# Optimization experiments

Measured on AMD Instinct MI355X. Metric: run time of the kernel, lower is better.

The kernel has to match this reference:

```python
import jax, jax.numpy as jnp
import numpy as np
import math

B, S, IN_DIM = 8, 1024, 64
OUT_DIM, NB = 128, 6
LN_EPS = 1e-5

def setup_inputs() -> dict:
    key = jax.random.key(0)
    k1, k2, k3, k4 = jax.random.split(key, 4)
    seq = jax.random.normal(k1, (B, S, IN_DIM), dtype=jnp.float32)
    # torch inits: M ~ U(-0.5,0.5), P ~ U(-0.1,0.1), residual_proj.weight ~ U(-0.1,0.1)
    M = jax.random.uniform(k2, (OUT_DIM, IN_DIM), minval=-0.5, maxval=0.5, dtype=jnp.float32)
    P = jax.random.uniform(k3, (OUT_DIM, OUT_DIM, NB), minval=-0.1, maxval=0.1, dtype=jnp.float32)
    res_W = jax.random.uniform(k4, (OUT_DIM, IN_DIM), minval=-0.1, maxval=0.1, dtype=jnp.float32)
    gamma = jnp.ones((OUT_DIM,), dtype=jnp.float32)
    beta = jnp.zeros((OUT_DIM,), dtype=jnp.float32)
    return {"seq": seq, "M": M, "P": P, "res_W": res_W, "gamma": gamma, "beta": beta}

def _layer(x, M, P, res_W, gamma, beta):
    b, s, _ = x.shape
    out_dim, _, nb = P.shape
    # x_trans = x @ M.T then LayerNorm over last dim
    x_t = jnp.einsum('bsj,ij->bsi', x, M)  # (b,s,out)
    mu = jnp.mean(x_t, axis=-1, keepdims=True)
    var = jnp.mean((x_t - mu) ** 2, axis=-1, keepdims=True)
    x_n = (x_t - mu) * jax.lax.rsqrt(var + LN_EPS) * gamma + beta
    # periods[i,j,g] = i*(out*nb) + j*nb + g + 2
    periods = (jnp.arange(out_dim * out_dim * nb, dtype=jnp.float32) + 2.0).reshape(out_dim, out_dim, nb)
    pos = jnp.arange(s, dtype=jnp.float32)
    phi = jnp.cos((2.0 * math.pi) * pos[:, None, None, None] / periods[None])  # (s,out,out,nb)
    # Nk[b,s,i] = sum_{j,g} P[i,j,g] * x_n[b,s,j] * phi[s,i,j,g]
    W = jnp.einsum('ijg,sijg->sij', P, phi)      # (s,out,out) position-dependent mixing
    Nk = jnp.einsum('bsj,sij->bsi', x_n, W)      # (b,s,out)
    residual = jnp.einsum('bsj,ij->bsi', x, res_W)  # 'separate' residual projection
    return Nk + residual

def reference(seq, M, P, res_W, gamma, beta):
    return _layer(seq, M, P, res_W, gamma, beta)
```

## Files before the change

kernel.cpp:

```cpp
#include <hip/hip_runtime.h>
#include <math.h>

#define BD 8
#define SD 1024
#define ID 64
#define OD 128
#define NBD 6
#define TI 4
#define SCH 32
#define SS 8
#define WPAD 136

typedef short bf16x8 __attribute__((ext_vector_type(8)));
typedef float f32x4 __attribute__((ext_vector_type(4)));
typedef ushort ushortx8 __attribute__((ext_vector_type(8)));

__device__ __forceinline__ ushort rne_bf16(float f) {
    union { float f; unsigned u; } cv; cv.f = f;
    return (ushort)((cv.u + 0x7FFFu + ((cv.u >> 16) & 1u)) >> 16);
}
__device__ __forceinline__ float bf16_to_f(ushort u) {
    union { unsigned u; float f; } cv; cv.u = ((unsigned)u) << 16;
    return cv.f;
}

__device__ __forceinline__ bf16x8 pack8(float4 a, float4 b) {
    union { ushort u[8]; bf16x8 v; } p;
    p.u[0] = rne_bf16(a.x); p.u[1] = rne_bf16(a.y);
    p.u[2] = rne_bf16(a.z); p.u[3] = rne_bf16(a.w);
    p.u[4] = rne_bf16(b.x); p.u[5] = rne_bf16(b.y);
    p.u[6] = rne_bf16(b.z); p.u[7] = rne_bf16(b.w);
    return p.v;
}

__device__ __forceinline__ void pack8_split(float4 a, float4 b,
                                            bf16x8* hi, bf16x8* lo) {
    union { ushort u[8]; bf16x8 v; } ph, pl;
    const float e[8] = {a.x, a.y, a.z, a.w, b.x, b.y, b.z, b.w};
    #pragma unroll
    for (int k = 0; k < 8; ++k) {
        const ushort h = rne_bf16(e[k]);
        ph.u[k] = h;
        pl.u[k] = rne_bf16(e[k] - bf16_to_f(h));
    }
    *hi = ph.v; *lo = pl.v;
}

__global__ __launch_bounds__(256) void ln_mfma(
    const float* __restrict__ seq,
    const float* __restrict__ M,
    const float* __restrict__ resW,
    const float* __restrict__ gamma,
    const float* __restrict__ beta,
    ushort* __restrict__ xnT,
    float* __restrict__ out)
{
    const int t  = threadIdx.x;
    const int s0 = blockIdx.x * 2;
    const int w  = t >> 6;
    const int l  = t & 63;
    const int lr = l & 15;
    const int lk = l >> 4;

    __shared__ float Ct[16][132];

    bf16x8 ahi[2], alo[2];
    {
        const int ba = lr & 7, sa = lr >> 3;
        const float* __restrict__ arow = &seq[(ba * SD + s0 + sa) * ID];
        #pragma unroll
        for (int ka = 0; ka < 2; ++ka) {
            const float4 v0 = *(const float4*)&arow[ka * 32 + lk * 8];
            const float4 v1 = *(const float4*)&arow[ka * 32 + lk * 8 + 4];
            pack8_split(v0, v1, &ahi[ka], &alo[ka]);
        }
    }
    bf16x8 bfr[2][2][2];
    #pragma unroll
    for (int mat = 0; mat < 2; ++mat) {
        const float* __restrict__ Wm = mat ? resW : M;
        #pragma unroll
        for (int ct = 0; ct < 2; ++ct) {
            const float* __restrict__ wrow = &Wm[(w * 32 + ct * 16 + lr) * ID];
            #pragma unroll
            for (int kb = 0; kb < 2; ++kb) {
                const float4 v0 = *(const float4*)&wrow[kb * 32 + lk * 8];
                const float4 v1 = *(const float4*)&wrow[kb * 32 + lk * 8 + 4];
                bfr[mat][ct][kb] = pack8(v0, v1);
            }
        }
    }

    f32x4 accx[2], accr[2];
    #pragma unroll
    for (int ct = 0; ct < 2; ++ct) {
        f32x4 a4 = {0.f, 0.f, 0.f, 0.f};
        a4 = __builtin_amdgcn_mfma_f32_16x16x32_bf16(alo[0], bfr[0][ct][0], a4, 0, 0, 0);
        a4 = __builtin_amdgcn_mfma_f32_16x16x32_bf16(alo[1], bfr[0][ct][1], a4, 0, 0, 0);
        a4 = __builtin_amdgcn_mfma_f32_16x16x32_bf16(ahi[0], bfr[0][ct][0], a4, 0, 0, 0);
        a4 = __builtin_amdgcn_mfma_f32_16x16x32_bf16(ahi[1], bfr[0][ct][1], a4, 0, 0, 0);
        accx[ct] = a4;
        f32x4 r4 = {0.f, 0.f, 0.f, 0.f};
        r4 = __builtin_amdgcn_mfma_f32_16x16x32_bf16(ahi[0], bfr[1][ct][0], r4, 0, 0, 0);
        r4 = __builtin_amdgcn_mfma_f32_16x16x32_bf16(ahi[1], bfr[1][ct][1], r4, 0, 0, 0);
        accr[ct] = r4;
    }

    #pragma unroll
    for (int ct = 0; ct < 2; ++ct)
        #pragma unroll
        for (int q = 0; q < 4; ++q) {
            const int r = lk * 4 + q;
            const int b = r & 7, sl = r >> 3;
            out[(b * SD + s0 + sl) * OD + w * 32 + ct * 16 + lr] = accr[ct][q];
        }
    #pragma unroll
    for (int ct = 0; ct < 2; ++ct)
        #pragma unroll
        for (int q = 0; q < 4; ++q)
            Ct[lk * 4 + q][w * 32 + ct * 16 + lr] = accx[ct][q];
    __syncthreads();

    {
        const int row = t >> 4;
        const int c0  = (t & 15) * 8;
        float sum = 0.f, ssq = 0.f;
        #pragma unroll
        for (int e = 0; e < 8; ++e) {
            const float v = Ct[row][c0 + e];
            sum += v; ssq = fmaf(v, v, ssq);
        }
        #pragma unroll
        for (int m = 1; m < 16; m <<= 1) {
            sum += __shfl_xor(sum, m, 64);
            ssq += __shfl_xor(ssq, m, 64);
        }
        const float mu   = sum * (1.0f / OD);
        const float vr   = ssq * (1.0f / OD) - mu * mu;
        const float rstd = rsqrtf(vr + 1e-5f);

        const float4 g0 = *(const float4*)&gamma[c0];
        const float4 g1 = *(const float4*)&gamma[c0 + 4];
        const float4 b0 = *(const float4*)&beta[c0];
        const float4 b1 = *(const float4*)&beta[c0 + 4];
        const float gv[8] = {g0.x,g0.y,g0.z,g0.w,g1.x,g1.y,g1.z,g1.w};
        const float bv[8] = {b0.x,b0.y,b0.z,b0.w,b1.x,b1.y,b1.z,b1.w};

        union { ushort u[8]; ushortx8 v; } xo;
        #pragma unroll
        for (int e = 0; e < 8; ++e) {
            const float xv = (Ct[row][c0 + e] - mu) * rstd * gv[e] + bv[e];
            xo.u[e] = rne_bf16(xv);
        }
        const int b  = row & 7, sl = row >> 3;
        *(ushortx8*)&xnT[((s0 + sl) * BD + b) * OD + c0] = xo.v;
    }
}

__global__ __launch_bounds__(512, 6) void nk_kernel(
    const float* __restrict__ P,
    const ushort* __restrict__ xnT,
    float* __restrict__ out)
{
    const int sc = blockIdx.x;
    const int i0 = blockIdx.y * TI;
    const int t  = threadIdx.x;
    const int iw = t >> 7;
    const int jb = t & 127;
    const int wv = t >> 6;
    const int l  = t & 63;

    __shared__ ushort Wl[SS][TI][WPAD];
    __shared__ ushort Xl[SS][BD][WPAD];
    __shared__ float  Cst[SS][BD][TI];

    float Pv[NBD], kk[NBD], c0[NBD], c1[NBD];
    const int ig = i0 + iw;
    const float s0f = (float)(sc * SCH);
    #pragma unroll
    for (int g = 0; g < NBD; ++g) {
        Pv[g] = P[(ig * OD + jb) * NBD + g];
        const float per = (float)(ig * (OD * NBD) + jb * NBD + g + 2);
        const float rp  = __builtin_amdgcn_rcpf(per);
        kk[g] = 2.0f * __builtin_amdgcn_cosf(rp);
        c1[g] = __builtin_amdgcn_cosf(__builtin_amdgcn_fractf(s0f * rp));
        c0[g] = __builtin_amdgcn_cosf(__builtin_amdgcn_fractf((s0f - 1.0f) * rp));
    }

    for (int u = 0; u < SCH / SS; ++u) {
        const int sb = sc * SCH + u * SS;
        {
            const uint4* __restrict__ src = (const uint4*)(xnT + sb * (BD * OD));
            #pragma unroll
            for (int r = 0; r < 2; ++r) {
                const int e  = t + 512 * r;
                const uint4 v = src[e];
                const int eo = e << 3;
                const int si = eo >> 10;
                const int b  = (eo >> 7) & 7;
                const int j0 = eo & 127;
                *(uint4*)&Xl[si][b][j0] = v;
            }
        }
        #pragma unroll
        for (int ssi = 0; ssi < SS; ++ssi) {
            float wvv = 0.f;
            #pragma unroll
            for (int g = 0; g < NBD; ++g) wvv = fmaf(Pv[g], c1[g], wvv);
            #pragma unroll
            for (int g = 0; g < NBD; ++g) {
                const float cn = fmaf(kk[g], c1[g], -c0[g]);
                c0[g] = c1[g]; c1[g] = cn;
            }
            Wl[ssi][iw][jb] = rne_bf16(wvv);
        }
        __syncthreads();
        {
            f32x4 acc4 = {0.f, 0.f, 0.f, 0.f};
            #pragma unroll
            for (int m = 0; m < 4; ++m) {
                const bf16x8 a = *(const bf16x8*)&Xl[wv][l & 7][m * 32 + (l >> 4) * 8];
                const bf16x8 b = *(const bf16x8*)&Wl[wv][l & 3][m * 32 + (l >> 4) * 8];
                acc4 = __builtin_amdgcn_mfma_f32_16x16x32_bf16(a, b, acc4, 0, 0, 0);
            }
            const int col  = l & 15;
            const int rowg = l >> 4;
            if (col < TI && rowg < 2) {
                #pragma unroll
                for (int q = 0; q < 4; ++q)
                    Cst[wv][rowg * 4 + q][col] = acc4[q];
            }
        }
        __syncthreads();
        if (t < SS * BD * TI) {
            const int ii  = t & 3;
            const int b   = (t >> 2) & 7;
            const int sl2 = t >> 5;
            out[(b * SD + sb + sl2) * OD + i0 + ii] += Cst[sl2][b][ii];
        }
        __syncthreads();
    }
}

extern "C" void kernel_launch(void* const* d_in, const int* in_sizes, int n_in,
                              void* d_out, int out_size, void* d_ws, size_t ws_size,
                              hipStream_t stream) {
    const float* seq   = (const float*)d_in[0];
    const float* M     = (const float*)d_in[1];
    const float* P     = (const float*)d_in[2];
    const float* resW  = (const float*)d_in[3];
    const float* gamma = (const float*)d_in[4];
    const float* beta  = (const float*)d_in[5];
    float* out = (float*)d_out;

    ushort* xnT = (ushort*)d_ws;

    ln_mfma<<<dim3(SD / 2), dim3(256), 0, stream>>>(seq, M, resW, gamma, beta,
                                                    xnT, out);
    nk_kernel<<<dim3(SD / SCH, OD / TI), dim3(512), 0, stream>>>(P, xnT, out);
}
```

Baseline: 26.36 us.

## Double-buffer X tiles and defer output accumulation to drop a barrier

Double-buffers the Xl shared-memory tile in nk_kernel. The next chunk's xnT is loaded from global memory into registers early in each iteration and written to the alternate buffer after the MFMA. The read-modify-write of out for the previous chunk is moved to the start of the next iteration, which removes one __syncthreads per loop. This is meant to hide global load latency and barrier stalls, at the cost of more shared memory (lower occupancy is possible) and extra registers for the prefetch.

```diff
diff --git a/kernel.cpp b/kernel.cpp
--- a/kernel.cpp
+++ b/kernel.cpp
@@ -10,6 +10,7 @@
 #define SCH 32
 #define SS 8
 #define WPAD 136
+#define NU (SCH / SS)
 
 typedef short bf16x8 __attribute__((ext_vector_type(8)));
 typedef float f32x4 __attribute__((ext_vector_type(4)));
@@ -170,8 +171,8 @@
     const int wv = t >> 6;
     const int l  = t & 63;
 
+    __shared__ ushort Xl[2][SS][BD][WPAD];
     __shared__ ushort Wl[SS][TI][WPAD];
-    __shared__ ushort Xl[SS][BD][WPAD];
     __shared__ float  Cst[SS][BD][TI];
 
     float Pv[NBD], kk[NBD], c0[NBD], c1[NBD];
@@ -187,20 +188,33 @@
         c0[g] = __builtin_amdgcn_cosf(__builtin_amdgcn_fractf((s0f - 1.0f) * rp));
     }
 
-    for (int u = 0; u < SCH / SS; ++u) {
-        const int sb = sc * SCH + u * SS;
-        {
-            const uint4* __restrict__ src = (const uint4*)(xnT + sb * (BD * OD));
-            #pragma unroll
-            for (int r = 0; r < 2; ++r) {
-                const int e  = t + 512 * r;
-                const uint4 v = src[e];
-                const int eo = e << 3;
-                const int si = eo >> 10;
-                const int b  = (eo >> 7) & 7;
-                const int j0 = eo & 127;
-                *(uint4*)&Xl[si][b][j0] = v;
-            }
+    const int e0  = t,        e1  = t + 512;
+    const int si0 = (e0 << 3) >> 10, b0 = ((e0 << 3) >> 7) & 7, j00 = (e0 << 3) & 127;
+    const int si1 = (e1 << 3) >> 10, b1 = ((e1 << 3) >> 7) & 7, j01 = (e1 << 3) & 127;
+
+    {
+        const uint4* __restrict__ src = (const uint4*)(xnT + (sc * SCH) * (BD * OD));
+        const uint4 v0 = src[e0];
+        const uint4 v1 = src[e1];
+        *(uint4*)&Xl[0][si0][b0][j00] = v0;
+        *(uint4*)&Xl[0][si1][b1][j01] = v1;
+    }
+
+    uint4 pf0, pf1;
+    for (int u = 0; u < NU; ++u) {
+        const int sb  = sc * SCH + u * SS;
+        const int cur = u & 1;
+
+        if (u + 1 < NU) {
+            const uint4* __restrict__ src = (const uint4*)(xnT + (sb + SS) * (BD * OD));
+            pf0 = src[e0];
+            pf1 = src[e1];
+        }
+        if (u > 0 && t < SS * BD * TI) {
+            const int ii  = t & 3;
+            const int b   = (t >> 2) & 7;
+            const int sl2 = t >> 5;
+            out[(b * SD + (sb - SS) + sl2) * OD + i0 + ii] += Cst[sl2][b][ii];
         }
         #pragma unroll
         for (int ssi = 0; ssi < SS; ++ssi) {
@@ -215,11 +229,12 @@
             Wl[ssi][iw][jb] = rne_bf16(wvv);
         }
         __syncthreads();
+
         {
             f32x4 acc4 = {0.f, 0.f, 0.f, 0.f};
             #pragma unroll
             for (int m = 0; m < 4; ++m) {
-                const bf16x8 a = *(const bf16x8*)&Xl[wv][l & 7][m * 32 + (l >> 4) * 8];
+                const bf16x8 a = *(const bf16x8*)&Xl[cur][wv][l & 7][m * 32 + (l >> 4) * 8];
                 const bf16x8 b = *(const bf16x8*)&Wl[wv][l & 3][m * 32 + (l >> 4) * 8];
                 acc4 = __builtin_amdgcn_mfma_f32_16x16x32_bf16(a, b, acc4, 0, 0, 0);
             }
@@ -231,14 +246,18 @@
                     Cst[wv][rowg * 4 + q][col] = acc4[q];
             }
         }
+        if (u + 1 < NU) {
+            *(uint4*)&Xl[cur ^ 1][si0][b0][j00] = pf0;
+            *(uint4*)&Xl[cur ^ 1][si1][b1][j01] = pf1;
+        }
         __syncthreads();
-        if (t < SS * BD * TI) {
-            const int ii  = t & 3;
-            const int b   = (t >> 2) & 7;
-            const int sl2 = t >> 5;
-            out[(b * SD + sb + sl2) * OD + i0 + ii] += Cst[sl2][b][ii];
-        }
-        __syncthreads();
+    }
+
+    if (t < SS * BD * TI) {
+        const int ii  = t & 3;
+        const int b   = (t >> 2) & 7;
+        const int sl2 = t >> 5;
+        out[(b * SD + sc * SCH + (NU - 1) * SS + sl2) * OD + i0 + ii] += Cst[sl2][b][ii];
     }
 }
 
```

After: 27.07 us. +2.7%, slower.

## Precompute position-dependent mixing weights in LN kernel, apply via per-position MFMA

Applied to the files above, without the earlier changes.

Moves the generation of the position-dependent mixing matrix W out of the apply kernel into extra blocks of the LayerNorm kernel, which write W as bf16 to a global workspace (32 MB). A new apply kernel then processes one sequence position per block, loading the full 128x128 W slice from global memory and doing a full-width MFMA over all output channels. This removes the per-tile recomputation and the multi-step sync loop, and lets W generation overlap with the LayerNorm work. In exchange it adds a large round trip of W through HBM and depends on workspace size.

```diff
diff --git a/kernel.cpp b/kernel.cpp
--- a/kernel.cpp
+++ b/kernel.cpp
@@ -6,9 +6,9 @@
 #define ID 64
 #define OD 128
 #define NBD 6
-#define TI 4
+#define LNB 512
+#define WGB 2048
 #define SCH 32
-#define SS 8
 #define WPAD 136
 
 typedef short bf16x8 __attribute__((ext_vector_type(8)));
@@ -23,7 +23,6 @@
     union { unsigned u; float f; } cv; cv.u = ((unsigned)u) << 16;
     return cv.f;
 }
-
 __device__ __forceinline__ bf16x8 pack8(float4 a, float4 b) {
     union { ushort u[8]; bf16x8 v; } p;
     p.u[0] = rne_bf16(a.x); p.u[1] = rne_bf16(a.y);
@@ -32,7 +31,6 @@
     p.u[6] = rne_bf16(b.z); p.u[7] = rne_bf16(b.w);
     return p.v;
 }
-
 __device__ __forceinline__ void pack8_split(float4 a, float4 b,
                                             bf16x8* hi, bf16x8* lo) {
     union { ushort u[8]; bf16x8 v; } ph, pl;
@@ -46,16 +44,53 @@
     *hi = ph.v; *lo = pl.v;
 }
 
-__global__ __launch_bounds__(256) void ln_mfma(
+__global__ __launch_bounds__(256) void ln_wgen(
     const float* __restrict__ seq,
     const float* __restrict__ M,
+    const float* __restrict__ P,
     const float* __restrict__ resW,
     const float* __restrict__ gamma,
     const float* __restrict__ beta,
     ushort* __restrict__ xnT,
+    ushort* __restrict__ Wt,
     float* __restrict__ out)
 {
-    const int t  = threadIdx.x;
+    const int t = threadIdx.x;
+
+    if (blockIdx.x >= LNB) {
+        const int idx = (blockIdx.x - LNB) * 256 + t;
+        const int j  = idx & 127;
+        const int i  = (idx >> 7) & 127;
+        const int st = idx >> 14;
+        const int s0 = st * SCH;
+
+        float Pv[NBD], kk[NBD], c0[NBD], c1[NBD];
+        const float s0f = (float)s0;
+        #pragma unroll
+        for (int g = 0; g < NBD; ++g) {
+            Pv[g] = P[(i * OD + j) * NBD + g];
+            const float per = (float)(i * (OD * NBD) + j * NBD + g + 2);
+            const float rp  = __builtin_amdgcn_rcpf(per);
+            kk[g] = 2.0f * __builtin_amdgcn_cosf(rp);
+            c1[g] = __builtin_amdgcn_cosf(__builtin_amdgcn_fractf(s0f * rp));
+            c0[g] = __builtin_amdgcn_cosf(__builtin_amdgcn_fractf((s0f - 1.0f) * rp));
+        }
+        ushort* __restrict__ wp = Wt + s0 * (OD * OD) + i * OD + j;
+        #pragma unroll 4
+        for (int ss = 0; ss < SCH; ++ss) {
+            float w = 0.f;
+            #pragma unroll
+            for (int g = 0; g < NBD; ++g) w = fmaf(Pv[g], c1[g], w);
+            wp[ss * (OD * OD)] = rne_bf16(w);
+            #pragma unroll
+            for (int g = 0; g < NBD; ++g) {
+                const float cn = fmaf(kk[g], c1[g], -c0[g]);
+                c0[g] = c1[g]; c1[g] = cn;
+            }
+        }
+        return;
+    }
+
     const int s0 = blockIdx.x * 2;
     const int w  = t >> 6;
     const int l  = t & 63;
@@ -157,88 +192,51 @@
     }
 }
 
-__global__ __launch_bounds__(512, 6) void nk_kernel(
-    const float* __restrict__ P,
+__global__ __launch_bounds__(512, 8) void apply_kernel(
+    const ushort* __restrict__ Wt,
     const ushort* __restrict__ xnT,
     float* __restrict__ out)
 {
-    const int sc = blockIdx.x;
-    const int i0 = blockIdx.y * TI;
+    const int s  = blockIdx.x;
     const int t  = threadIdx.x;
-    const int iw = t >> 7;
-    const int jb = t & 127;
     const int wv = t >> 6;
     const int l  = t & 63;
 
-    __shared__ ushort Wl[SS][TI][WPAD];
-    __shared__ ushort Xl[SS][BD][WPAD];
-    __shared__ float  Cst[SS][BD][TI];
-
-    float Pv[NBD], kk[NBD], c0[NBD], c1[NBD];
-    const int ig = i0 + iw;
-    const float s0f = (float)(sc * SCH);
-    #pragma unroll
-    for (int g = 0; g < NBD; ++g) {
-        Pv[g] = P[(ig * OD + jb) * NBD + g];
-        const float per = (float)(ig * (OD * NBD) + jb * NBD + g + 2);
-        const float rp  = __builtin_amdgcn_rcpf(per);
-        kk[g] = 2.0f * __builtin_amdgcn_cosf(rp);
-        c1[g] = __builtin_amdgcn_cosf(__builtin_amdgcn_fractf(s0f * rp));
-        c0[g] = __builtin_amdgcn_cosf(__builtin_amdgcn_fractf((s0f - 1.0f) * rp));
-    }
-
-    for (int u = 0; u < SCH / SS; ++u) {
-        const int sb = sc * SCH + u * SS;
-        {
-            const uint4* __restrict__ src = (const uint4*)(xnT + sb * (BD * OD));
-            #pragma unroll
-            for (int r = 0; r < 2; ++r) {
-                const int e  = t + 512 * r;
-                const uint4 v = src[e];
-                const int eo = e << 3;
-                const int si = eo >> 10;
-                const int b  = (eo >> 7) & 7;
-                const int j0 = eo & 127;
-                *(uint4*)&Xl[si][b][j0] = v;
-            }
-        }
-        #pragma unroll
-        for (int ssi = 0; ssi < SS; ++ssi) {
-            float wvv = 0.f;
-            #pragma unroll
-            for (int g = 0; g < NBD; ++g) wvv = fmaf(Pv[g], c1[g], wvv);
-            #pragma unroll
-            for (int g = 0; g < NBD; ++g) {
-                const float cn = fmaf(kk[g], c1[g], -c0[g]);
-                c0[g] = c1[g]; c1[g] = cn;
-            }
-            Wl[ssi][iw][jb] = rne_bf16(wvv);
-        }
-        __syncthreads();
-        {
-            f32x4 acc4 = {0.f, 0.f, 0.f, 0.f};
-            #pragma unroll
-            for (int m = 0; m < 4; ++m) {
-                const bf16x8 a = *(const bf16x8*)&Xl[wv][l & 7][m * 32 + (l >> 4) * 8];
-                const bf16x8 b = *(const bf16x8*)&Wl[wv][l & 3][m * 32 + (l >> 4) * 8];
-                acc4 = __builtin_amdgcn_mfma_f32_16x16x32_bf16(a, b, acc4, 0, 0, 0);
-            }
-            const int col  = l & 15;
-            const int rowg = l >> 4;
-            if (col < TI && rowg < 2) {
-                #pragma unroll
-                for (int q = 0; q < 4; ++q)
-                    Cst[wv][rowg * 4 + q][col] = acc4[q];
-            }
-        }
-        __syncthreads();
-        if (t < SS * BD * TI) {
-            const int ii  = t & 3;
-            const int b   = (t >> 2) & 7;
-            const int sl2 = t >> 5;
-            out[(b * SD + sb + sl2) * OD + i0 + ii] += Cst[sl2][b][ii];
-        }
-        __syncthreads();
+    __shared__ ushort Xl[BD][WPAD];
+
+    if (t < 128) {
+        const uint4 v = ((const uint4*)(xnT + s * (BD * OD)))[t];
+        const int b = t >> 4, j0 = (t & 15) * 8;
+        *(uint4*)&Xl[b][j0] = v;
+    }
+    __syncthreads();
+
+    const ushort* __restrict__ wrow =
+        Wt + s * (OD * OD) + (wv * 16 + (l & 15)) * OD + (l >> 4) * 8;
+    bf16x8 bf0 = *(const bf16x8*)&wrow[0];
+    bf16x8 bf1 = *(const bf16x8*)&wrow[32];
+    bf16x8 bf2 = *(const bf16x8*)&wrow[64];
+    bf16x8 bf3 = *(const bf16x8*)&wrow[96];
+
+    const bf16x8 af0 = *(const bf16x8*)&Xl[l & 7][0  + (l >> 4) * 8];
+    const bf16x8 af1 = *(const bf16x8*)&Xl[l & 7][32 + (l >> 4) * 8];
+    const bf16x8 af2 = *(const bf16x8*)&Xl[l & 7][64 + (l >> 4) * 8];
+    const bf16x8 af3 = *(const bf16x8*)&Xl[l & 7][96 + (l >> 4) * 8];
+
+    f32x4 acc = {0.f, 0.f, 0.f, 0.f};
+    acc = __builtin_amdgcn_mfma_f32_16x16x32_bf16(af0, bf0, acc, 0, 0, 0);
+    acc = __builtin_amdgcn_mfma_f32_16x16x32_bf16(af1, bf1, acc, 0, 0, 0);
+    acc = __builtin_amdgcn_mfma_f32_16x16x32_bf16(af2, bf2, acc, 0, 0, 0);
+    acc = __builtin_amdgcn_mfma_f32_16x16x32_bf16(af3, bf3, acc, 0, 0, 0);
+
+    const int col  = l & 15;
+    const int rowg = l >> 4;
+    if (rowg < 2) {
+        #pragma unroll
+        for (int q = 0; q < 4; ++q) {
+            const int b = rowg * 4 + q;
+            out[(b * SD + s) * OD + wv * 16 + col] += acc[q];
+        }
     }
 }
 
@@ -254,8 +252,9 @@
     float* out = (float*)d_out;
 
     ushort* xnT = (ushort*)d_ws;
-
-    ln_mfma<<<dim3(SD / 2), dim3(256), 0, stream>>>(seq, M, resW, gamma, beta,
-                                                    xnT, out);
-    nk_kernel<<<dim3(SD / SCH, OD / TI), dim3(512), 0, stream>>>(P, xnT, out);
-}
+    ushort* Wt  = xnT + SD * BD * OD;
+
+    ln_wgen<<<dim3(LNB + WGB), dim3(256), 0, stream>>>(
+        seq, M, P, resW, gamma, beta, xnT, Wt, out);
+    apply_kernel<<<dim3(SD), dim3(512), 0, stream>>>(Wt, xnT, out);
+}
```

Result: slower. 34.42 us (+30.6%).
